# Kernel optimization log

Measured on AMD Instinct MI355X. Metric: run time of the kernel, lower is better.

## Reference

```python
import jax, jax.numpy as jnp
import numpy as np
import math

B, L, D = 256, 64, 1024
H, MAXREL = 16, 32
HD = D // H            # 64
HG = H // 2            # 8 heads in global MHA
HDG = D // HG          # 128


def setup_inputs() -> dict:
    key = jax.random.key(0)
    ks = jax.random.split(key, 16)
    s = 0.02
    inp = {
        'query': jax.random.normal(ks[0], (B, L, D), jnp.float32),
        'key':   jax.random.normal(ks[1], (B, L, D), jnp.float32),
        'value': jax.random.normal(ks[2], (B, L, D), jnp.float32),
        # local attention projections
        'Wq': jax.random.normal(ks[3], (D, D), jnp.float32) * s,
        'bq': jnp.zeros((D,), jnp.float32),
        'Wk': jax.random.normal(ks[4], (D, D), jnp.float32) * s,
        'bk': jnp.zeros((D,), jnp.float32),
        'Wv': jax.random.normal(ks[5], (D, D), jnp.float32) * s,
        'bv': jnp.zeros((D,), jnp.float32),
        'Wo': jax.random.normal(ks[6], (D, D), jnp.float32) * s,
        'bo': jnp.zeros((D,), jnp.float32),
        # relative position embedding tables (2*MAXREL+1, head_dim)
        'rel_k': jax.random.normal(ks[7], (2 * MAXREL + 1, HD), jnp.float32) * s,
        'rel_v': jax.random.normal(ks[8], (2 * MAXREL + 1, HD), jnp.float32) * s,
        # torch nn.MultiheadAttention params: packed in_proj (3D, D) and out_proj
        'g_in_w': jax.random.normal(ks[9], (3 * D, D), jnp.float32) * s,
        'g_in_b': jnp.zeros((3 * D,), jnp.float32),
        'g_out_w': jax.random.normal(ks[10], (D, D), jnp.float32) * s,
        'g_out_b': jnp.zeros((D,), jnp.float32),
    }
    return inp


def _forward(query, key, value, Wq, bq, Wk, bk, Wv, bv, Wo, bo,
             rel_k, rel_v, g_in_w, g_in_b, g_out_w, g_out_b):
    # ---- local attention with relative position bias ----
    q = (query @ Wq.T + bq).reshape(B, L, H, HD).transpose(0, 2, 1, 3)  # [B,H,L,hd]
    k = (key   @ Wk.T + bk).reshape(B, L, H, HD).transpose(0, 2, 1, 3)
    v = (value @ Wv.T + bv).reshape(B, L, H, HD).transpose(0, 2, 1, 3)

    scale = math.sqrt(HD)
    scores = jnp.einsum('bhld,bhmd->bhlm', q, k) / scale  # [B,H,L,L]

    # relative positions: dist[l, r] = clip(r - l, -MAXREL, MAXREL) + MAXREL
    # (only applied because L <= 2*MAXREL, matching the torch condition)
    rng = jnp.arange(L)
    rel_ids = jnp.clip(rng[None, :] - rng[:, None], -MAXREL, MAXREL) + MAXREL
    rel_pos_k = rel_k[rel_ids]  # [L, L, hd]; rel_v is looked up but unused upstream
    scores = scores + jnp.einsum('bhld,lrd->bhlr', q, rel_pos_k)

    attn = jax.nn.softmax(scores, axis=-1)  # dropout is identity in eval
    local = jnp.einsum('bhlm,bhmd->bhld', attn, v)
    local = local.transpose(0, 2, 1, 3).reshape(B, L, D)

    # ---- global branch: standard torch MultiheadAttention (8 heads) ----
    Wq_g, Wk_g, Wv_g = jnp.split(g_in_w, 3, axis=0)
    bq_g, bk_g, bv_g = jnp.split(g_in_b, 3, axis=0)
    qg = (query @ Wq_g.T + bq_g).reshape(B, L, HG, HDG).transpose(0, 2, 1, 3)
    kg = (key   @ Wk_g.T + bk_g).reshape(B, L, HG, HDG).transpose(0, 2, 1, 3)
    vg = (value @ Wv_g.T + bv_g).reshape(B, L, HG, HDG).transpose(0, 2, 1, 3)
    sg = jnp.einsum('bhld,bhmd->bhlm', qg, kg) / math.sqrt(HDG)
    ag = jax.nn.softmax(sg, axis=-1)
    glob = jnp.einsum('bhlm,bhmd->bhld', ag, vg).transpose(0, 2, 1, 3).reshape(B, L, D)
    glob = glob @ g_out_w.T + g_out_b

    combined = 0.7 * local + 0.3 * glob
    return combined @ Wo.T + bo


def reference(query, key, value, Wq, bq, Wk, bk, Wv, bv, Wo, bo,
              rel_k, rel_v, g_in_w, g_in_b, g_out_w, g_out_b):
    return _forward(query, key, value, Wq, bq, Wk, bk, Wv, bv, Wo, bo,
                    rel_k, rel_v, g_in_w, g_in_b, g_out_w, g_out_b)
```

## Files before the change

kernel.cpp:

```cpp
#include <hip/hip_runtime.h>
#include <hip/hip_bf16.h>

typedef __hip_bfloat16 bf16;
typedef __bf16  bf16x8 __attribute__((ext_vector_type(8)));
typedef float   f32x4  __attribute__((ext_vector_type(4)));

#define BL    16384
#define DDIM  1024
#define NREL  65

#define GLOBAL_AS(p) ((const __attribute__((address_space(1))) void*)(p))
#define LDS_AS(p)    ((__attribute__((address_space(3))) void*)(p))

#define MFMA16(a, b, c) __builtin_amdgcn_mfma_f32_16x16x32_bf16((a), (b), (c), 0, 0, 0)

__global__ __launch_bounds__(256) void cvt_f32_bf16(const float* __restrict__ in,
                                                    bf16* __restrict__ out, int n)
{
    int i = (blockIdx.x * 256 + threadIdx.x) * 4;
    if (i >= n) return;
    float4 v = *(const float4*)(in + i);
    union { bf16 h[4]; uint2 u; } o;
    o.h[0] = __float2bfloat16(v.x);
    o.h[1] = __float2bfloat16(v.y);
    o.h[2] = __float2bfloat16(v.z);
    o.h[3] = __float2bfloat16(v.w);
    *(uint2*)(out + i) = o.u;
}

__global__ __launch_bounds__(256) void blend_kernel(const bf16* __restrict__ a,
                                                    const bf16* __restrict__ b,
                                                    bf16* __restrict__ out, int n)
{
    int i = (blockIdx.x * 256 + threadIdx.x) * 4;
    if (i >= n) return;
    union { bf16 h[4]; uint2 u; } ua, ub, o;
    ua.u = *(const uint2*)(a + i);
    ub.u = *(const uint2*)(b + i);
#pragma unroll
    for (int k = 0; k < 4; ++k)
        o.h[k] = __float2bfloat16(0.7f * __bfloat162float(ua.h[k]) +
                                  0.3f * __bfloat162float(ub.h[k]));
    *(uint2*)(out + i) = o.u;
}

template <typename TC>
__global__ __launch_bounds__(512, 2) void gemm256(
    const bf16* __restrict__ A,
    const bf16* __restrict__ W0, const bf16* __restrict__ W1,
    const float* __restrict__ bias0, const float* __restrict__ bias1,
    TC* __restrict__ C0, TC* __restrict__ C1,
    int M, int K, int NX, int NSPLIT)
{
    __shared__ __align__(16) char smem[131072];
    bf16* const A0 = (bf16*)smem;
    bf16* const A1 = (bf16*)(smem + 32768);
    bf16* const B0 = (bf16*)(smem + 65536);
    bf16* const B1 = (bf16*)(smem + 98304);

    const int t    = threadIdx.x;
    const int w    = t >> 6;
    const int lane = t & 63;
    const int m    = lane & 15;
    const int g4   = lane >> 4;
    const int wr   = w >> 2;
    const int wcn  = w & 3;

    const int nwg = gridDim.x;
    const int q8 = nwg >> 3, r8 = nwg & 7;
    const int xcd = blockIdx.x & 7, loc = blockIdx.x >> 3;
    const int wg = (xcd < r8 ? xcd * (q8 + 1) : r8 * (q8 + 1) + (xcd - r8) * q8) + loc;
    const int rowBase = (wg / NX) * 256;
    const int colBase = (wg % NX) * 256;

    const bf16* Wp; const float* bs; TC* Cp; int colW;
    if (colBase < NSPLIT) {
        Wp = W0 + (size_t)colBase * K; bs = bias0 + colBase; Cp = C0; colW = colBase;
    } else {
        Wp = W1 + (size_t)(colBase - NSPLIT) * K;
        bs = bias1 + (colBase - NSPLIT); Cp = C1; colW = colBase - NSPLIT;
    }

    const char* Ab = (const char*)A + (size_t)rowBase * (size_t)(K * 2);
    const char* Wb = (const char*)Wp;
    const int ldb  = K * 2;
    const int rsub = lane >> 3;
    const int swz  = ((lane & 7) << 4) ^ (rsub << 4);

    auto stage = [&](bf16* Ad, bf16* Bd, int kt) {
        const int ktb = kt * 128;
#pragma unroll
        for (int s = 0; s < 4; ++s) {
            const int row = w * 32 + s * 8;
            __builtin_amdgcn_global_load_lds(
                GLOBAL_AS(Ab + (size_t)(row + rsub) * ldb + ktb + swz),
                LDS_AS(Ad + row * 64), 16, 0, 0);
        }
#pragma unroll
        for (int s = 0; s < 4; ++s) {
            const int row = w * 32 + s * 8;
            __builtin_amdgcn_global_load_lds(
                GLOBAL_AS(Wb + (size_t)(row + rsub) * ldb + ktb + swz),
                LDS_AS(Bd + row * 64), 16, 0, 0);
        }
    };

    f32x4 acc[8][4] = {};
    const int NT = K >> 6;

    stage(A0, B0, 0);
    stage(A1, B1, 1);

    const int ar0  = wr * 128;
    const int br0  = wcn * 64;
    const int cswz = (m & 7) << 4;

    for (int tt = 0; tt < NT; ++tt) {
        const char* Ac = (const char*)((tt & 1) ? A1 : A0);
        const char* Bc = (const char*)((tt & 1) ? B1 : B0);
        if (tt < NT - 1) asm volatile("s_waitcnt vmcnt(8)" ::: "memory");
        else             asm volatile("s_waitcnt vmcnt(0)" ::: "memory");
        __builtin_amdgcn_s_barrier();
        __builtin_amdgcn_sched_barrier(0);

        bf16x8 af[8], bfA[4], bfB[4];
#pragma unroll
        for (int i = 0; i < 4; ++i)
#pragma unroll
            for (int kk = 0; kk < 2; ++kk)
                af[i*2+kk] = *(const bf16x8*)(Ac + (ar0 + i*16 + m) * 128 +
                                              ((kk*64 + g4*16) ^ cswz));
#pragma unroll
        for (int j = 0; j < 2; ++j)
#pragma unroll
            for (int kk = 0; kk < 2; ++kk)
                bfA[j*2+kk] = *(const bf16x8*)(Bc + (br0 + j*16 + m) * 128 +
                                               ((kk*64 + g4*16) ^ cswz));
        __builtin_amdgcn_s_setprio(1);
#pragma unroll
        for (int i = 0; i < 4; ++i)
#pragma unroll
            for (int j = 0; j < 2; ++j)
#pragma unroll
                for (int kk = 0; kk < 2; ++kk)
                    acc[i][j] = MFMA16(af[i*2+kk], bfA[j*2+kk], acc[i][j]);
        __builtin_amdgcn_s_setprio(0);
#pragma unroll
        for (int j = 0; j < 2; ++j)
#pragma unroll
            for (int kk = 0; kk < 2; ++kk)
                bfB[j*2+kk] = *(const bf16x8*)(Bc + (br0 + (j+2)*16 + m) * 128 +
                                               ((kk*64 + g4*16) ^ cswz));
        __builtin_amdgcn_s_setprio(1);
#pragma unroll
        for (int i = 0; i < 4; ++i)
#pragma unroll
            for (int j = 0; j < 2; ++j)
#pragma unroll
                for (int kk = 0; kk < 2; ++kk)
                    acc[i][j+2] = MFMA16(af[i*2+kk], bfB[j*2+kk], acc[i][j+2]);
        __builtin_amdgcn_s_setprio(0);
#pragma unroll
        for (int i = 0; i < 4; ++i)
#pragma unroll
            for (int kk = 0; kk < 2; ++kk)
                af[i*2+kk] = *(const bf16x8*)(Ac + (ar0 + 64 + i*16 + m) * 128 +
                                              ((kk*64 + g4*16) ^ cswz));
        __builtin_amdgcn_s_setprio(1);
#pragma unroll
        for (int i = 0; i < 4; ++i)
#pragma unroll
            for (int j = 0; j < 2; ++j)
#pragma unroll
                for (int kk = 0; kk < 2; ++kk)
                    acc[4+i][j+2] = MFMA16(af[i*2+kk], bfB[j*2+kk], acc[4+i][j+2]);
#pragma unroll
        for (int i = 0; i < 4; ++i)
#pragma unroll
            for (int j = 0; j < 2; ++j)
#pragma unroll
                for (int kk = 0; kk < 2; ++kk)
                    acc[4+i][j] = MFMA16(af[i*2+kk], bfA[j*2+kk], acc[4+i][j]);
        __builtin_amdgcn_s_setprio(0);

        __builtin_amdgcn_s_barrier();
        __builtin_amdgcn_sched_barrier(0);
        if (tt + 2 < NT) stage((tt & 1) ? A1 : A0, (tt & 1) ? B1 : B0, tt + 2);
    }

    float bv[4];
#pragma unroll
    for (int j = 0; j < 4; ++j) bv[j] = bs[wcn * 64 + j * 16 + m];

    if constexpr (sizeof(TC) == 2) {
        __syncthreads();
        bf16* Cs = (bf16*)smem;
#pragma unroll
        for (int i = 0; i < 8; ++i)
#pragma unroll
            for (int j = 0; j < 4; ++j)
#pragma unroll
                for (int r = 0; r < 4; ++r)
                    Cs[(wr*128 + i*16 + g4*4 + r) * 256 + wcn*64 + j*16 + m] =
                        __float2bfloat16(acc[i][j][r] + bv[j]);
        __syncthreads();
        char* Cb = (char*)Cp + (size_t)rowBase * (size_t)(NSPLIT * 2) + (size_t)colW * 2;
#pragma unroll
        for (int p = 0; p < 16; ++p) {
            const int row = p * 16 + (t >> 5);
            const int cbt = (t & 31) * 16;
            *(uint4*)(Cb + (size_t)row * (size_t)(NSPLIT * 2) + cbt) =
                *(const uint4*)(smem + row * 512 + cbt);
        }
    } else {
        float* Cf = (float*)Cp;
#pragma unroll
        for (int j = 0; j < 4; ++j) {
            const int col = colW + wcn*64 + j*16 + m;
#pragma unroll
            for (int i = 0; i < 8; ++i)
#pragma unroll
                for (int r = 0; r < 4; ++r)
                    Cf[(size_t)(rowBase + wr*128 + i*16 + g4*4 + r) * NSPLIT + col] =
                        acc[i][j][r] + bv[j];
        }
    }
}

__global__ __launch_bounds__(256) void local_attn_mfma(
    const bf16* __restrict__ Q, const bf16* __restrict__ K,
    const bf16* __restrict__ V, const float* __restrict__ RelK,
    bf16* __restrict__ Out)
{
    __shared__ __align__(16) bf16 qs[64 * 64];
    __shared__ __align__(16) bf16 ks[64 * 64];
    __shared__ __align__(16) bf16 rs[80 * 64];
    __shared__ __align__(16) bf16 vt[64 * 66];
    __shared__ __align__(16) bf16 qrl[64 * 80];
    __shared__ __align__(16) bf16 ps[64 * 64];

    const int t    = threadIdx.x;
    const int lane = t & 63;
    const int wv   = t >> 6;
    const int m    = lane & 15;
    const int g4   = lane >> 4;
    const int b    = blockIdx.x >> 4;
    const int h    = blockIdx.x & 15;
    const size_t base = (size_t)b * 64 * DDIM + (size_t)h * 64;

    for (int i = t; i < 1024; i += 256) {
        int e = i * 4, l = e >> 6, d = e & 63;
        const size_t g = base + (size_t)l * DDIM + d;
        *(uint2*)(qs + l * 64 + d) = *(const uint2*)(Q + g);
        *(uint2*)(ks + l * 64 + d) = *(const uint2*)(K + g);
        const bf16* vp = V + g;
        vt[(d + 0) * 66 + l] = vp[0];
        vt[(d + 1) * 66 + l] = vp[1];
        vt[(d + 2) * 66 + l] = vp[2];
        vt[(d + 3) * 66 + l] = vp[3];
    }
    for (int i = t; i < NREL * 64; i += 256)
        rs[i] = __float2bfloat16(RelK[i]);
    __syncthreads();

    bf16x8 af[2];
    af[0] = *(const bf16x8*)(qs + (wv * 16 + m) * 64 + 0  + g4 * 8);
    af[1] = *(const bf16x8*)(qs + (wv * 16 + m) * 64 + 32 + g4 * 8);
    f32x4 accS[4] = {}, accR[5] = {};
#pragma unroll
    for (int j = 0; j < 4; ++j)
#pragma unroll
        for (int kc = 0; kc < 2; ++kc) {
            bf16x8 bk = *(const bf16x8*)(ks + (j * 16 + m) * 64 + kc * 32 + g4 * 8);
            accS[j] = MFMA16(af[kc], bk, accS[j]);
        }
#pragma unroll
    for (int p = 0; p < 5; ++p)
#pragma unroll
        for (int kc = 0; kc < 2; ++kc) {
            bf16x8 br = *(const bf16x8*)(rs + (p * 16 + m) * 64 + kc * 32 + g4 * 8);
            accR[p] = MFMA16(af[kc], br, accR[p]);
        }
#pragma unroll
    for (int p = 0; p < 5; ++p)
#pragma unroll
        for (int r = 0; r < 4; ++r)
            qrl[(wv * 16 + g4 * 4 + r) * 80 + p * 16 + m] = __float2bfloat16(accR[p][r]);
    __syncthreads();

    float sc[4][4];
#pragma unroll
    for (int j = 0; j < 4; ++j) {
        const int c = j * 16 + m;
#pragma unroll
        for (int r = 0; r < 4; ++r) {
            const int l = wv * 16 + g4 * 4 + r;
            int rel = c - l;
            rel = rel < -32 ? -32 : (rel > 32 ? 32 : rel);
            sc[j][r] = accS[j][r] * 0.125f +
                       __bfloat162float(qrl[l * 80 + rel + 32]);
        }
    }
#pragma unroll
    for (int r = 0; r < 4; ++r) {
        float mx = fmaxf(fmaxf(sc[0][r], sc[1][r]), fmaxf(sc[2][r], sc[3][r]));
        mx = fmaxf(mx, __shfl_xor(mx, 1));
        mx = fmaxf(mx, __shfl_xor(mx, 2));
        mx = fmaxf(mx, __shfl_xor(mx, 4));
        mx = fmaxf(mx, __shfl_xor(mx, 8));
        float s = 0.f;
#pragma unroll
        for (int j = 0; j < 4; ++j) { float e = __expf(sc[j][r] - mx); sc[j][r] = e; s += e; }
        s += __shfl_xor(s, 1); s += __shfl_xor(s, 2);
        s += __shfl_xor(s, 4); s += __shfl_xor(s, 8);
        const float inv = 1.f / s;
#pragma unroll
        for (int j = 0; j < 4; ++j)
            ps[(wv * 16 + g4 * 4 + r) * 64 + j * 16 + m] = __float2bfloat16(sc[j][r] * inv);
    }
    __syncthreads();

    bf16x8 pf[2];
    pf[0] = *(const bf16x8*)(ps + (wv * 16 + m) * 64 + 0  + g4 * 8);
    pf[1] = *(const bf16x8*)(ps + (wv * 16 + m) * 64 + 32 + g4 * 8);
    f32x4 accO[4] = {};
#pragma unroll
    for (int j = 0; j < 4; ++j)
#pragma unroll
        for (int kc = 0; kc < 2; ++kc) {
            union { bf16x8 v; unsigned short u[8]; } bu;
            const unsigned short* vp =
                (const unsigned short*)vt + (j * 16 + m) * 66 + kc * 32 + g4 * 8;
#pragma unroll
            for (int c = 0; c < 8; ++c) bu.u[c] = vp[c];
            accO[j] = MFMA16(pf[kc], bu.v, accO[j]);
        }
#pragma unroll
    for (int j = 0; j < 4; ++j)
#pragma unroll
        for (int r = 0; r < 4; ++r)
            Out[base + (size_t)(wv * 16 + g4 * 4 + r) * DDIM + j * 16 + m] =
                __float2bfloat16(accO[j][r]);
}

__global__ __launch_bounds__(256) void global_attn_mfma(
    const bf16* Qg, const bf16* __restrict__ Kg,
    const bf16* __restrict__ Vg, bf16* Out)
{
    __shared__ __align__(16) bf16 qs[64 * 136];
    __shared__ __align__(16) bf16 ks[64 * 136];
    __shared__ __align__(16) bf16 vt[128 * 66];
    __shared__ __align__(16) bf16 ps[64 * 64];

    const int t    = threadIdx.x;
    const int lane = t & 63;
    const int wv   = t >> 6;
    const int m    = lane & 15;
    const int g4   = lane >> 4;
    const int b    = blockIdx.x >> 3;
    const int hg   = blockIdx.x & 7;
    const size_t base = (size_t)b * 64 * DDIM + (size_t)hg * 128;

    for (int i = t; i < 2048; i += 256) {
        int e = i * 4, l = e >> 7, d = e & 127;
        const size_t g = base + (size_t)l * DDIM + d;
        *(uint2*)(qs + l * 136 + d) = *(const uint2*)(Qg + g);
        *(uint2*)(ks + l * 136 + d) = *(const uint2*)(Kg + g);
        const bf16* vp = Vg + g;
        vt[(d + 0) * 66 + l] = vp[0];
        vt[(d + 1) * 66 + l] = vp[1];
        vt[(d + 2) * 66 + l] = vp[2];
        vt[(d + 3) * 66 + l] = vp[3];
    }
    __syncthreads();

    bf16x8 af[4];
#pragma unroll
    for (int kc = 0; kc < 4; ++kc)
        af[kc] = *(const bf16x8*)(qs + (wv * 16 + m) * 136 + kc * 32 + g4 * 8);
    f32x4 accS[4] = {};
#pragma unroll
    for (int j = 0; j < 4; ++j)
#pragma unroll
        for (int kc = 0; kc < 4; ++kc) {
            bf16x8 bk = *(const bf16x8*)(ks + (j * 16 + m) * 136 + kc * 32 + g4 * 8);
            accS[j] = MFMA16(af[kc], bk, accS[j]);
        }

    float sc[4][4];
#pragma unroll
    for (int j = 0; j < 4; ++j)
#pragma unroll
        for (int r = 0; r < 4; ++r)
            sc[j][r] = accS[j][r] * 0.08838834764831845f;
#pragma unroll
    for (int r = 0; r < 4; ++r) {
        float mx = fmaxf(fmaxf(sc[0][r], sc[1][r]), fmaxf(sc[2][r], sc[3][r]));
        mx = fmaxf(mx, __shfl_xor(mx, 1));
        mx = fmaxf(mx, __shfl_xor(mx, 2));
        mx = fmaxf(mx, __shfl_xor(mx, 4));
        mx = fmaxf(mx, __shfl_xor(mx, 8));
        float s = 0.f;
#pragma unroll
        for (int j = 0; j < 4; ++j) { float e = __expf(sc[j][r] - mx); sc[j][r] = e; s += e; }
        s += __shfl_xor(s, 1); s += __shfl_xor(s, 2);
        s += __shfl_xor(s, 4); s += __shfl_xor(s, 8);
        const float inv = 1.f / s;
#pragma unroll
        for (int j = 0; j < 4; ++j)
            ps[(wv * 16 + g4 * 4 + r) * 64 + j * 16 + m] = __float2bfloat16(sc[j][r] * inv);
    }
    __syncthreads();

    bf16x8 pf[2];
    pf[0] = *(const bf16x8*)(ps + (wv * 16 + m) * 64 + 0  + g4 * 8);
    pf[1] = *(const bf16x8*)(ps + (wv * 16 + m) * 64 + 32 + g4 * 8);
    f32x4 accO[8] = {};
#pragma unroll
    for (int j = 0; j < 8; ++j)
#pragma unroll
        for (int kc = 0; kc < 2; ++kc) {
            union { bf16x8 v; unsigned short u[8]; } bu;
            const unsigned short* vp =
                (const unsigned short*)vt + (j * 16 + m) * 66 + kc * 32 + g4 * 8;
#pragma unroll
            for (int c = 0; c < 8; ++c) bu.u[c] = vp[c];
            accO[j] = MFMA16(pf[kc], bu.v, accO[j]);
        }
#pragma unroll
    for (int j = 0; j < 8; ++j)
#pragma unroll
        for (int r = 0; r < 4; ++r)
            Out[base + (size_t)(wv * 16 + g4 * 4 + r) * DDIM + j * 16 + m] =
                __float2bfloat16(accO[j][r]);
}

extern "C" void kernel_launch(void* const* d_in, const int* in_sizes, int n_in,
                              void* d_out, int out_size, void* d_ws, size_t ws_size,
                              hipStream_t stream)
{
    const float* query   = (const float*)d_in[0];
    const float* key     = (const float*)d_in[1];
    const float* value   = (const float*)d_in[2];
    const float* Wq      = (const float*)d_in[3];
    const float* bq      = (const float*)d_in[4];
    const float* Wk      = (const float*)d_in[5];
    const float* bk      = (const float*)d_in[6];
    const float* Wv      = (const float*)d_in[7];
    const float* bv      = (const float*)d_in[8];
    const float* Wo      = (const float*)d_in[9];
    const float* bo      = (const float*)d_in[10];
    const float* rel_k   = (const float*)d_in[11];
    const float* g_in_w  = (const float*)d_in[13];
    const float* g_in_b  = (const float*)d_in[14];
    const float* g_out_w = (const float*)d_in[15];
    const float* g_out_b = (const float*)d_in[16];

    char* ws = (char*)d_ws;
    const size_t SZ = (size_t)BL * DDIM * sizeof(bf16);
    const size_t MM = (size_t)DDIM * DDIM;
    const size_t WB = 8 * MM * sizeof(bf16);
    const bool big = ws_size >= 6 * SZ + WB;
    const int nslots = big ? 6 : 5;

    bf16* s0 = (bf16*)(ws + 0 * SZ);
    bf16* s1 = (bf16*)(ws + 1 * SZ);
    bf16* s2 = (bf16*)(ws + 2 * SZ);
    bf16* s3 = (bf16*)(ws + 3 * SZ);
    bf16* s4 = (bf16*)(ws + 4 * SZ);
    bf16* s5 = (bf16*)(ws + 5 * SZ);
    bf16* wb = (bf16*)(ws + nslots * SZ);
    bf16* wgq = wb;
    bf16* wgk = wb + 1 * MM;
    bf16* wgv = wb + 2 * MM;
    bf16* wq  = wb + 3 * MM;
    bf16* wk  = wb + 4 * MM;
    bf16* wvw = wb + 5 * MM;
    bf16* wo  = wb + 6 * MM;
    bf16* wgo = wb + 7 * MM;

    float* out = (float*)d_out;

    dim3 blk(256);
    dim3 blkG(512);
    const int nAct = BL * DDIM;
    dim3 gCvtA(nAct / 1024);
    dim3 gCvtW((int)MM / 1024);
    dim3 gCvtG(3 * (int)MM / 1024);
    dim3 gLocal(256 * 16);
    dim3 gGlobal(256 * 8);
    dim3 gFus(512);
    dim3 gUnf(256);

    cvt_f32_bf16<<<gCvtG, blk, 0, stream>>>(g_in_w, wgq, 3 * (int)MM);
    cvt_f32_bf16<<<gCvtW, blk, 0, stream>>>(Wq, wq, (int)MM);
    cvt_f32_bf16<<<gCvtW, blk, 0, stream>>>(Wk, wk, (int)MM);
    cvt_f32_bf16<<<gCvtW, blk, 0, stream>>>(Wv, wvw, (int)MM);
    cvt_f32_bf16<<<gCvtW, blk, 0, stream>>>(Wo, wo, (int)MM);
    cvt_f32_bf16<<<gCvtW, blk, 0, stream>>>(g_out_w, wgo, (int)MM);

    if (big) {
        cvt_f32_bf16<<<gCvtA, blk, 0, stream>>>(query, s0, nAct);
        cvt_f32_bf16<<<gCvtA, blk, 0, stream>>>(key,   s1, nAct);
        cvt_f32_bf16<<<gCvtA, blk, 0, stream>>>(value, s2, nAct);

        bf16* vscr = (bf16*)d_out;

        gemm256<bf16><<<gFus, blkG, 0, stream>>>(s0, wgq, wq,  g_in_b,        bq, s3, s4,
                                                 BL, DDIM, 8, DDIM);
        gemm256<bf16><<<gFus, blkG, 0, stream>>>(s1, wgk, wk,  g_in_b + 1024, bk, s5, s0,
                                                 BL, DDIM, 8, DDIM);
        gemm256<bf16><<<gFus, blkG, 0, stream>>>(s2, wgv, wvw, g_in_b + 2048, bv, vscr, s1,
                                                 BL, DDIM, 8, DDIM);

        global_attn_mfma<<<gGlobal, blk, 0, stream>>>(s3, s5, vscr, s3);
        gemm256<bf16><<<gUnf, blkG, 0, stream>>>(s3, wgo, wgo, g_out_b, g_out_b, s5, s5,
                                                 BL, DDIM, 4, DDIM);

        local_attn_mfma<<<gLocal, blk, 0, stream>>>(s4, s0, s1, rel_k, s2);

        blend_kernel<<<gCvtA, blk, 0, stream>>>(s2, s5, s0, nAct);
        gemm256<float><<<gUnf, blkG, 0, stream>>>(s0, wo, wo, bo, bo, out, out,
                                                  BL, DDIM, 4, DDIM);
    } else {
        cvt_f32_bf16<<<gCvtA, blk, 0, stream>>>(query, s0, nAct);
        gemm256<bf16><<<gUnf, blkG, 0, stream>>>(s0, wgq, wgq, g_in_b, g_in_b, s1, s1,
                                                 BL, DDIM, 4, DDIM);
        cvt_f32_bf16<<<gCvtA, blk, 0, stream>>>(key, s0, nAct);
        gemm256<bf16><<<gUnf, blkG, 0, stream>>>(s0, wgk, wgk, g_in_b + 1024, g_in_b + 1024,
                                                 s2, s2, BL, DDIM, 4, DDIM);
        cvt_f32_bf16<<<gCvtA, blk, 0, stream>>>(value, s0, nAct);
        gemm256<bf16><<<gUnf, blkG, 0, stream>>>(s0, wgv, wgv, g_in_b + 2048, g_in_b + 2048,
                                                 s3, s3, BL, DDIM, 4, DDIM);

        global_attn_mfma<<<gGlobal, blk, 0, stream>>>(s1, s2, s3, s4);
        gemm256<bf16><<<gUnf, blkG, 0, stream>>>(s4, wgo, wgo, g_out_b, g_out_b, s1, s1,
                                                 BL, DDIM, 4, DDIM);

        cvt_f32_bf16<<<gCvtA, blk, 0, stream>>>(query, s0, nAct);
        gemm256<bf16><<<gUnf, blkG, 0, stream>>>(s0, wq, wq, bq, bq, s2, s2,
                                                 BL, DDIM, 4, DDIM);
        cvt_f32_bf16<<<gCvtA, blk, 0, stream>>>(key, s0, nAct);
        gemm256<bf16><<<gUnf, blkG, 0, stream>>>(s0, wk, wk, bk, bk, s3, s3,
                                                 BL, DDIM, 4, DDIM);
        cvt_f32_bf16<<<gCvtA, blk, 0, stream>>>(value, s0, nAct);
        gemm256<bf16><<<gUnf, blkG, 0, stream>>>(s0, wvw, wvw, bv, bv, s4, s4,
                                                 BL, DDIM, 4, DDIM);

        local_attn_mfma<<<gLocal, blk, 0, stream>>>(s2, s3, s4, rel_k, s0);

        blend_kernel<<<gCvtA, blk, 0, stream>>>(s0, s1, s2, nAct);
        gemm256<float><<<gUnf, blkG, 0, stream>>>(s2, wo, wo, bo, bo, out, out,
                                                  BL, DDIM, 4, DDIM);
    }
}
```

Before: 695.9 us.

## Interleave next-tile global-to-LDS loads with MFMA phases, one barrier per iteration

The GEMM main loop now prefetches one tile ahead instead of two. The global-to-LDS copies for tile tt+1 are split into four parts, each placed between the LDS fragment reads and MFMA groups of the current tile, with sched_barriers holding the order. Each iteration ends with a single waitcnt plus barrier instead of a barrier at both ends. The B fragment is reloaded from LDS for the last phase, which lowers register pressure but costs extra LDS reads. The shorter prefetch distance may expose more global-load latency.

```diff
diff --git a/kernel.cpp b/kernel.cpp
--- a/kernel.cpp
+++ b/kernel.cpp
@@ -13,6 +13,7 @@
 #define LDS_AS(p)    ((__attribute__((address_space(3))) void*)(p))
 
 #define MFMA16(a, b, c) __builtin_amdgcn_mfma_f32_16x16x32_bf16((a), (b), (c), 0, 0, 0)
+#define SB0() __builtin_amdgcn_sched_barrier(0)
 
 __global__ __launch_bounds__(256) void cvt_f32_bf16(const float* __restrict__ in,
                                                     bf16* __restrict__ out, int n)
@@ -87,29 +88,25 @@
     const int rsub = lane >> 3;
     const int swz  = ((lane & 7) << 4) ^ (rsub << 4);
 
-    auto stage = [&](bf16* Ad, bf16* Bd, int kt) {
+    auto stagePart = [&](bf16* Ad, bf16* Bd, int kt, int s) {
         const int ktb = kt * 128;
-#pragma unroll
-        for (int s = 0; s < 4; ++s) {
-            const int row = w * 32 + s * 8;
-            __builtin_amdgcn_global_load_lds(
-                GLOBAL_AS(Ab + (size_t)(row + rsub) * ldb + ktb + swz),
-                LDS_AS(Ad + row * 64), 16, 0, 0);
-        }
-#pragma unroll
-        for (int s = 0; s < 4; ++s) {
-            const int row = w * 32 + s * 8;
-            __builtin_amdgcn_global_load_lds(
-                GLOBAL_AS(Wb + (size_t)(row + rsub) * ldb + ktb + swz),
-                LDS_AS(Bd + row * 64), 16, 0, 0);
-        }
+        const int row = w * 32 + s * 8;
+        __builtin_amdgcn_global_load_lds(
+            GLOBAL_AS(Ab + (size_t)(row + rsub) * ldb + ktb + swz),
+            LDS_AS(Ad + row * 64), 16, 0, 0);
+        __builtin_amdgcn_global_load_lds(
+            GLOBAL_AS(Wb + (size_t)(row + rsub) * ldb + ktb + swz),
+            LDS_AS(Bd + row * 64), 16, 0, 0);
     };
 
     f32x4 acc[8][4] = {};
     const int NT = K >> 6;
 
-    stage(A0, B0, 0);
-    stage(A1, B1, 1);
+#pragma unroll
+    for (int s = 0; s < 4; ++s) stagePart(A0, B0, 0, s);
+    asm volatile("s_waitcnt vmcnt(0)" ::: "memory");
+    __builtin_amdgcn_s_barrier();
+    SB0();
 
     const int ar0  = wr * 128;
     const int br0  = wcn * 64;
@@ -118,74 +115,101 @@
     for (int tt = 0; tt < NT; ++tt) {
         const char* Ac = (const char*)((tt & 1) ? A1 : A0);
         const char* Bc = (const char*)((tt & 1) ? B1 : B0);
-        if (tt < NT - 1) asm volatile("s_waitcnt vmcnt(8)" ::: "memory");
-        else             asm volatile("s_waitcnt vmcnt(0)" ::: "memory");
-        __builtin_amdgcn_s_barrier();
-        __builtin_amdgcn_sched_barrier(0);
-
-        bf16x8 af[8], bfA[4], bfB[4];
+        bf16* const nAd = (tt & 1) ? A0 : A1;
+        bf16* const nBd = (tt & 1) ? B0 : B1;
+        const bool pf = (tt + 1 < NT);
+
+        bf16x8 a0[4][2], a1[4][2], b0[2][2], b1[2][2], b0b[2][2];
+
 #pragma unroll
         for (int i = 0; i < 4; ++i)
 #pragma unroll
-            for (int kk = 0; kk < 2; ++kk)
-                af[i*2+kk] = *(const bf16x8*)(Ac + (ar0 + i*16 + m) * 128 +
-                                              ((kk*64 + g4*16) ^ cswz));
+            for (int k = 0; k < 2; ++k)
+                a0[i][k] = *(const bf16x8*)(Ac + (ar0 + i*16 + m) * 128 +
+                                            ((k*64 + g4*16) ^ cswz));
 #pragma unroll
         for (int j = 0; j < 2; ++j)
 #pragma unroll
-            for (int kk = 0; kk < 2; ++kk)
-                bfA[j*2+kk] = *(const bf16x8*)(Bc + (br0 + j*16 + m) * 128 +
-                                               ((kk*64 + g4*16) ^ cswz));
+            for (int k = 0; k < 2; ++k)
+                b0[j][k] = *(const bf16x8*)(Bc + (br0 + j*16 + m) * 128 +
+                                            ((k*64 + g4*16) ^ cswz));
+        if (pf) stagePart(nAd, nBd, tt + 1, 0);
+
+#pragma unroll
+        for (int j = 0; j < 2; ++j)
+#pragma unroll
+            for (int k = 0; k < 2; ++k)
+                b1[j][k] = *(const bf16x8*)(Bc + (br0 + (j+2)*16 + m) * 128 +
+                                            ((k*64 + g4*16) ^ cswz));
+        if (pf) stagePart(nAd, nBd, tt + 1, 1);
+        SB0();
+
         __builtin_amdgcn_s_setprio(1);
 #pragma unroll
         for (int i = 0; i < 4; ++i)
 #pragma unroll
             for (int j = 0; j < 2; ++j)
 #pragma unroll
-                for (int kk = 0; kk < 2; ++kk)
-                    acc[i][j] = MFMA16(af[i*2+kk], bfA[j*2+kk], acc[i][j]);
+                for (int k = 0; k < 2; ++k)
+                    acc[i][j] = MFMA16(a0[i][k], b0[j][k], acc[i][j]);
         __builtin_amdgcn_s_setprio(0);
+        SB0();
+
+#pragma unroll
+        for (int i = 0; i < 4; ++i)
+#pragma unroll
+            for (int k = 0; k < 2; ++k)
+                a1[i][k] = *(const bf16x8*)(Ac + (ar0 + 64 + i*16 + m) * 128 +
+                                            ((k*64 + g4*16) ^ cswz));
+        if (pf) stagePart(nAd, nBd, tt + 1, 2);
+        SB0();
+
+        __builtin_amdgcn_s_setprio(1);
+#pragma unroll
+        for (int i = 0; i < 4; ++i)
+#pragma unroll
+            for (int j = 0; j < 2; ++j)
+#pragma unroll
+                for (int k = 0; k < 2; ++k)
+                    acc[i][j+2] = MFMA16(a0[i][k], b1[j][k], acc[i][j+2]);
+        __builtin_amdgcn_s_setprio(0);
+        SB0();
+
 #pragma unroll
         for (int j = 0; j < 2; ++j)
 #pragma unroll
-            for (int kk = 0; kk < 2; ++kk)
-                bfB[j*2+kk] = *(const bf16x8*)(Bc + (br0 + (j+2)*16 + m) * 128 +
-                                               ((kk*64 + g4*16) ^ cswz));
+            for (int k = 0; k < 2; ++k)
+                b0b[j][k] = *(const bf16x8*)(Bc + (br0 + j*16 + m) * 128 +
+                                             ((k*64 + g4*16) ^ cswz));
+        if (pf) stagePart(nAd, nBd, tt + 1, 3);
+        SB0();
+
         __builtin_amdgcn_s_setprio(1);
 #pragma unroll
         for (int i = 0; i < 4; ++i)
 #pragma unroll
             for (int j = 0; j < 2; ++j)
 #pragma unroll
-                for (int kk = 0; kk < 2; ++kk)
-                    acc[i][j+2] = MFMA16(af[i*2+kk], bfB[j*2+kk], acc[i][j+2]);
+                for (int k = 0; k < 2; ++k)
+                    acc[4+i][j+2] = MFMA16(a1[i][k], b1[j][k], acc[4+i][j+2]);
         __builtin_amdgcn_s_setprio(0);
+        SB0();
+
+        __builtin_amdgcn_s_setprio(1);
 #pragma unroll
         for (int i = 0; i < 4; ++i)
 #pragma unroll
-            for (int kk = 0; kk < 2; ++kk)
-                af[i*2+kk] = *(const bf16x8*)(Ac + (ar0 + 64 + i*16 + m) * 128 +
-                                              ((kk*64 + g4*16) ^ cswz));
-        __builtin_amdgcn_s_setprio(1);
-#pragma unroll
-        for (int i = 0; i < 4; ++i)
-#pragma unroll
             for (int j = 0; j < 2; ++j)
 #pragma unroll
-                for (int kk = 0; kk < 2; ++kk)
-                    acc[4+i][j+2] = MFMA16(af[i*2+kk], bfB[j*2+kk], acc[4+i][j+2]);
-#pragma unroll
-        for (int i = 0; i < 4; ++i)
-#pragma unroll
-            for (int j = 0; j < 2; ++j)
-#pragma unroll
-                for (int kk = 0; kk < 2; ++kk)
-                    acc[4+i][j] = MFMA16(af[i*2+kk], bfA[j*2+kk], acc[4+i][j]);
+                for (int k = 0; k < 2; ++k)
+                    acc[4+i][j] = MFMA16(a1[i][k], b0b[j][k], acc[4+i][j]);
         __builtin_amdgcn_s_setprio(0);
 
-        __builtin_amdgcn_s_barrier();
-        __builtin_amdgcn_sched_barrier(0);
-        if (tt + 2 < NT) stage((tt & 1) ? A1 : A0, (tt & 1) ? B1 : B0, tt + 2);
+        if (pf) {
+            asm volatile("s_waitcnt vmcnt(0)" ::: "memory");
+            __builtin_amdgcn_s_barrier();
+            SB0();
+        }
     }
 
     float bv[4];
```

Result: faster. 674.4 us (-3.1%).
